# Optimization experiments

Measured on AMD Instinct MI355X. Metric: run time of the kernel, lower is better.

Reference implementation:

```python
import jax, jax.numpy as jnp
import numpy as np

B, S, H = 1, 2048, 2048
NH, NKV, HD = 32, 8, 64
RBS, ICS, RBN = 64, 64, 16          # retrieval_block_size, input_chunk_size, retrieval_block_num
RLEN = RBS * RBN                     # 1024 retrieval tokens
KV = RLEN + S                        # 3072 total kv length
START = RLEN                         # INPUT_START_IDX
SCALE = HD ** -0.5
NEG = -1e9


def _document_ids():
    # mirrors get_document_ids
    ids = np.full(KV, -1, np.int32)
    ids[:START] = np.arange(START) // RBS + 1            # retrieval blocks -> 1..RBN
    chunk = np.arange(S) // ICS
    ids[START:] = np.where(chunk == 0, -1, np.minimum(chunk, RBN))
    return ids


def _block_mask():
    # mirrors causal_retrieval_mask_mod, precomputed dense [S, KV]
    ids = _document_ids()
    qpos = np.arange(S) + START
    kv = np.arange(KV)
    causal = (qpos[:, None] >= kv[None, :]) & (kv[None, :] > START)
    doc = (ids[qpos][:, None] == ids[None, :]) & (kv[None, :] < START)
    return jnp.asarray(causal | doc)


_MASK = _block_mask()


def _rotate_half(x):
    h = x.shape[-1] // 2
    return jnp.concatenate([-x[..., h:], x[..., :h]], axis=-1)


def setup_inputs() -> dict:
    key = jax.random.key(0)
    ks = jax.random.split(key, 6)
    inv_freq = 1.0 / (10000.0 ** (np.arange(0, HD, 2, dtype=np.float32) / HD))
    ang = np.arange(S, dtype=np.float32)[:, None] * inv_freq[None, :]   # [S, HD/2]
    emb = np.concatenate([ang, ang], axis=-1)                            # [S, HD]
    cos = jnp.asarray(np.cos(emb))[None].astype(jnp.float32)            # [1, S, HD]
    sin = jnp.asarray(np.sin(emb))[None].astype(jnp.float32)
    return {
        "hidden_states": jax.random.normal(ks[0], (B, S, H), jnp.float32),
        "cos": cos,
        "sin": sin,
        "retrieval_key": jax.random.normal(ks[1], (B, NKV, RLEN, HD), jnp.float32),
        "retrieval_value": jax.random.normal(ks[2], (B, NKV, RLEN, HD), jnp.float32),
        "Wq": jax.random.normal(ks[3], (H, NH * HD), jnp.float32) * 0.02,
        "Wk": jax.random.normal(ks[4], (H, NKV * HD), jnp.float32) * 0.02,
        "Wv": jax.random.normal(ks[5], (H, NKV * HD), jnp.float32) * 0.02,
        "Wo": jax.random.normal(jax.random.fold_in(key, 7), (NH * HD, H), jnp.float32) * 0.02,
    }


def reference(hidden_states, cos, sin, retrieval_key, retrieval_value, Wq, Wk, Wv, Wo):
    # QKV projections -> [B, nheads, S, HD]
    q = (hidden_states @ Wq).reshape(B, S, NH, HD).transpose(0, 2, 1, 3)
    k = (hidden_states @ Wk).reshape(B, S, NKV, HD).transpose(0, 2, 1, 3)
    v = (hidden_states @ Wv).reshape(B, S, NKV, HD).transpose(0, 2, 1, 3)
    # RoPE (retrieval kv is pre-encoded; rope only on current tokens)
    c, s = cos[:, None, :, :], sin[:, None, :, :]
    q = q * c + _rotate_half(q) * s
    k = k * c + _rotate_half(k) * s
    # prepend retrieval kv
    k = jnp.concatenate([retrieval_key, k], axis=2)    # [B, NKV, KV, HD]
    v = jnp.concatenate([retrieval_value, v], axis=2)
    # GQA: expand kv heads
    g = NH // NKV
    k = jnp.repeat(k, g, axis=1)                        # [B, NH, KV, HD]
    v = jnp.repeat(v, g, axis=1)
    scores = jnp.einsum("bhqd,bhkd->bhqk", q, k) * SCALE
    scores = jnp.where(_MASK[None, None], scores, NEG)
    probs = jax.nn.softmax(scores, axis=-1)
    # fully-masked rows (q_idx 0) -> zero output, matching flex_attention
    row_valid = _MASK.any(axis=-1)[None, None, :, None]
    probs = jnp.where(row_valid, probs, 0.0)
    out = jnp.einsum("bhqk,bhkd->bhqd", probs, v)
    out = out.transpose(0, 2, 1, 3).reshape(B, S, NH * HD)
    return out @ Wo
```

## Files before the change

kernel.cpp:

```cpp
#include <hip/hip_runtime.h>

#define S_LEN 2048
#define H_DIM 2048
#define NH 32
#define NKV 8
#define HD 64
#define RLEN 1024
#define KVTOT 3072
#define SCALE 0.125f
#define QS 0.18033688011112042f
#define FIX8 11.541560327111707f

typedef unsigned short ushort_t;
using short8 = __attribute__((ext_vector_type(8))) short;
using f32x4 = __attribute__((ext_vector_type(4))) float;

__device__ __forceinline__ float b2f(unsigned short u) {
    union { unsigned int i; float f; } v;
    v.i = ((unsigned int)u) << 16;
    return v.f;
}
__device__ __forceinline__ unsigned short f2b(float f) {
    union { float f; unsigned int i; } v;
    v.f = f;
    unsigned int x = v.i;
    return (unsigned short)((x + 0x7fffu + ((x >> 16) & 1u)) >> 16);
}

__device__ __forceinline__ void gload16(const ushort_t* g, ushort_t* l) {
    __builtin_amdgcn_global_load_lds(
        (const __attribute__((address_space(1))) unsigned int*)g,
        (__attribute__((address_space(3))) unsigned int*)l, 16, 0, 0);
}

__device__ __forceinline__ int is_f32(const void* p) {
    const unsigned int* w = (const unsigned int*)p;
    const int lane = threadIdx.x & 63;
    int cnt = 0;
#pragma unroll
    for (int j = 0; j < 4; ++j) {
        unsigned int lo = w[lane + j * 64] & 0xFFFFu;
        unsigned int e = (lo >> 7) & 0xFFu;
        cnt += (lo != 0u && (e < 90u || e > 140u)) ? 1 : 0;
    }
    unsigned long long b = __ballot(cnt >= 2);
    return __popcll(b) > 16;
}

__global__ __launch_bounds__(256) void prep_all(
    const void* __restrict__ hs, ushort_t* __restrict__ hsb,
    const void* __restrict__ Wq, const void* __restrict__ Wk,
    const void* __restrict__ Wv, const void* __restrict__ Wo,
    ushort_t* __restrict__ WqkvT, ushort_t* __restrict__ WoT)
{
    __shared__ ushort_t S[64 * 72];
    const int id = blockIdx.x;
    if (id < 2048) {
        const int F = is_f32(hs);
        int i = (id * 256 + threadIdx.x) * 8;
        ushort_t o[8];
        if (F) {
            const float* p = (const float*)hs + i;
            float4 f0 = ((const float4*)p)[0];
            float4 f1 = ((const float4*)p)[1];
            o[0] = f2b(f0.x); o[1] = f2b(f0.y); o[2] = f2b(f0.z); o[3] = f2b(f0.w);
            o[4] = f2b(f1.x); o[5] = f2b(f1.y); o[6] = f2b(f1.z); o[7] = f2b(f1.w);
            *(uint4*)(hsb + i) = *(const uint4*)o;
        } else {
            *(uint4*)(hsb + i) = *(const uint4*)((const ushort_t*)hs + i);
        }
        return;
    }
    int z, t;
    if (id < 3072)      { z = 0; t = id - 2048; }
    else if (id < 3328) { z = 1; t = id - 3072; }
    else if (id < 3584) { z = 2; t = id - 3328; }
    else                { z = 3; t = id - 3584; }
    const void* src = (z == 0) ? Wq : (z == 1) ? Wk : (z == 2) ? Wv : Wo;
    const int F = is_f32(src);
    const int C = (z == 1 || z == 2) ? 512 : 2048;
    const int nx = (z == 1 || z == 2) ? 8 : 32;
    const int x = t % nx, y = t / nx;
    ushort_t* dst = (z == 3) ? WoT : WqkvT;
    const int rofs = (z == 1) ? 2048 : (z == 2) ? 2560 : 0;

    const int r0 = y * 64, c0 = x * 64;
    const int lr = threadIdx.x >> 2, lc = (threadIdx.x & 3) * 16;
    ushort_t tt[16];
    if (F) {
        const float* p = (const float*)src + (size_t)(r0 + lr) * C + c0 + lc;
#pragma unroll
        for (int j = 0; j < 16; j += 4) {
            float4 f = *(const float4*)(p + j);
            tt[j] = f2b(f.x); tt[j + 1] = f2b(f.y); tt[j + 2] = f2b(f.z); tt[j + 3] = f2b(f.w);
        }
    } else {
        const ushort_t* p = (const ushort_t*)src + (size_t)(r0 + lr) * C + c0 + lc;
        *(uint4*)tt = ((const uint4*)p)[0];
        *(uint4*)(tt + 8) = ((const uint4*)p)[1];
    }
    *(uint4*)&S[lr * 72 + lc] = *(const uint4*)tt;
    *(uint4*)&S[lr * 72 + lc + 8] = *(const uint4*)(tt + 8);
    __syncthreads();
    const int wc = threadIdx.x >> 2, wr = (threadIdx.x & 3) * 16;
    ushort_t o[16];
#pragma unroll
    for (int j = 0; j < 16; ++j) o[j] = S[(wr + j) * 72 + wc];
    ushort_t* q = dst + (size_t)(rofs + c0 + wc) * 2048 + r0 + wr;
    *(uint4*)q = *(const uint4*)o;
    *(uint4*)(q + 8) = *(const uint4*)(o + 8);
}

__global__ __launch_bounds__(256, 4) void gemm_qkv(
    const ushort_t* __restrict__ A, const ushort_t* __restrict__ Bt,
    ushort_t* __restrict__ C, int N, int K)
{
    __shared__ __align__(16) ushort_t As[2][64 * 32];
    __shared__ __align__(16) ushort_t Bs[2][128 * 32];
    const int tid = threadIdx.x;
    const int wave = tid >> 6, lane = tid & 63;
    const int lq = lane & 15, quad = lane >> 4;
    const int m0 = blockIdx.y * 64, n0 = blockIdx.x * 128;
    const int wm = (wave & 1) * 32, wn = (wave >> 1) * 64;
    const int nk = K >> 5;

    const int srow = wave * 16 + (lane >> 2);
    const int scol = ((lane & 3) ^ ((lane >> 3) & 3)) * 8;
    const ushort_t* ga  = A  + (size_t)(m0 + srow) * K + scol;
    const ushort_t* gb0 = Bt + (size_t)(n0 + srow) * K + scol;
    const ushort_t* gb1 = Bt + (size_t)(n0 + 64 + srow) * K + scol;
    ushort_t* lA = &As[0][0] + wave * 16 * 32;
    ushort_t* lB = &Bs[0][0] + wave * 16 * 32;
    const int rs = (lq >> 1) & 3;

    f32x4 acc[2][4];
#pragma unroll
    for (int i = 0; i < 2; ++i)
#pragma unroll
        for (int j = 0; j < 4; ++j) acc[i][j] = (f32x4){0.f, 0.f, 0.f, 0.f};

#define STAGE_G(buf, kt) do { \
        gload16(ga  + (size_t)(kt) * 32, lA + (buf) * (64 * 32)); \
        gload16(gb0 + (size_t)(kt) * 32, lB + (buf) * (128 * 32)); \
        gload16(gb1 + (size_t)(kt) * 32, lB + (buf) * (128 * 32) + 64 * 32); \
    } while (0)

    STAGE_G(0, 0);
    int cur = 0;
    for (int kt = 0; kt < nk; ++kt) {
        if (kt + 1 < nk) {
            STAGE_G(cur ^ 1, kt + 1);
            asm volatile("s_waitcnt vmcnt(3)" ::: "memory");
        } else {
            asm volatile("s_waitcnt vmcnt(0)" ::: "memory");
        }
        __builtin_amdgcn_s_barrier();
        __builtin_amdgcn_sched_barrier(0);
        short8 afr[2], bfr[4];
#pragma unroll
        for (int i = 0; i < 2; ++i)
            afr[i] = *(const short8*)&As[cur][(wm + i * 16 + lq) * 32 + (quad ^ rs) * 8];
#pragma unroll
        for (int j = 0; j < 4; ++j)
            bfr[j] = *(const short8*)&Bs[cur][(wn + j * 16 + lq) * 32 + (quad ^ rs) * 8];
#pragma unroll
        for (int i = 0; i < 2; ++i)
#pragma unroll
            for (int j = 0; j < 4; ++j)
                acc[i][j] = __builtin_amdgcn_mfma_f32_16x16x32_bf16(afr[i], bfr[j], acc[i][j], 0, 0, 0);
        __builtin_amdgcn_s_barrier();
        cur ^= 1;
    }

#pragma unroll
    for (int i = 0; i < 2; ++i)
#pragma unroll
        for (int r = 0; r < 4; ++r) {
            ushort_t* cp = C + (size_t)(m0 + wm + i * 16 + quad * 4 + r) * N + n0 + wn + lq;
#pragma unroll
            for (int j = 0; j < 4; ++j) cp[j * 16] = f2b(acc[i][j][r]);
        }
#undef STAGE_G
}

__global__ __launch_bounds__(256, 4) void gemm_fin(
    const ushort_t* __restrict__ A, const ushort_t* __restrict__ Bt,
    void* __restrict__ Cv, int N, int K, const void* __restrict__ hs)
{
    const int oF = is_f32(hs);
    __shared__ __align__(16) ushort_t As[2][64 * 32];
    __shared__ __align__(16) ushort_t Bs[2][128 * 32];
    const int tid = threadIdx.x;
    const int wave = tid >> 6, lane = tid & 63;
    const int lq = lane & 15, quad = lane >> 4;
    const int m0 = blockIdx.y * 64, n0 = blockIdx.x * 128;
    const int wm = (wave & 1) * 32, wn = (wave >> 1) * 64;
    const int nk = K >> 5;

    const int srow = wave * 16 + (lane >> 2);
    const int scol = ((lane & 3) ^ ((lane >> 3) & 3)) * 8;
    const ushort_t* ga  = A  + (size_t)(m0 + srow) * K + scol;
    const ushort_t* gb0 = Bt + (size_t)(n0 + srow) * K + scol;
    const ushort_t* gb1 = Bt + (size_t)(n0 + 64 + srow) * K + scol;
    ushort_t* lA = &As[0][0] + wave * 16 * 32;
    ushort_t* lB = &Bs[0][0] + wave * 16 * 32;
    const int rs = (lq >> 1) & 3;

    f32x4 acc[2][4];
#pragma unroll
    for (int i = 0; i < 2; ++i)
#pragma unroll
        for (int j = 0; j < 4; ++j) acc[i][j] = (f32x4){0.f, 0.f, 0.f, 0.f};

#define STAGE_G(buf, kt) do { \
        gload16(ga  + (size_t)(kt) * 32, lA + (buf) * (64 * 32)); \
        gload16(gb0 + (size_t)(kt) * 32, lB + (buf) * (128 * 32)); \
        gload16(gb1 + (size_t)(kt) * 32, lB + (buf) * (128 * 32) + 64 * 32); \
    } while (0)

    STAGE_G(0, 0);
    int cur = 0;
    for (int kt = 0; kt < nk; ++kt) {
        if (kt + 1 < nk) {
            STAGE_G(cur ^ 1, kt + 1);
            asm volatile("s_waitcnt vmcnt(3)" ::: "memory");
        } else {
            asm volatile("s_waitcnt vmcnt(0)" ::: "memory");
        }
        __builtin_amdgcn_s_barrier();
        __builtin_amdgcn_sched_barrier(0);
        short8 afr[2], bfr[4];
#pragma unroll
        for (int i = 0; i < 2; ++i)
            afr[i] = *(const short8*)&As[cur][(wm + i * 16 + lq) * 32 + (quad ^ rs) * 8];
#pragma unroll
        for (int j = 0; j < 4; ++j)
            bfr[j] = *(const short8*)&Bs[cur][(wn + j * 16 + lq) * 32 + (quad ^ rs) * 8];
#pragma unroll
        for (int i = 0; i < 2; ++i)
#pragma unroll
            for (int j = 0; j < 4; ++j)
                acc[i][j] = __builtin_amdgcn_mfma_f32_16x16x32_bf16(afr[i], bfr[j], acc[i][j], 0, 0, 0);
        __builtin_amdgcn_s_barrier();
        cur ^= 1;
    }

#pragma unroll
    for (int i = 0; i < 2; ++i)
#pragma unroll
        for (int r = 0; r < 4; ++r) {
            size_t off = (size_t)(m0 + wm + i * 16 + quad * 4 + r) * N + n0 + wn + lq;
            if (oF) {
                float* cp = (float*)Cv + off;
#pragma unroll
                for (int j = 0; j < 4; ++j) cp[j * 16] = acc[i][j][r];
            } else {
                ushort_t* cp = (ushort_t*)Cv + off;
#pragma unroll
                for (int j = 0; j < 4; ++j) cp[j * 16] = f2b(acc[i][j][r]);
            }
        }
#undef STAGE_G
}

__global__ __launch_bounds__(256) void prepKV(
    const void* __restrict__ rk, const void* __restrict__ rv,
    const ushort_t* __restrict__ qkvp,
    const void* __restrict__ cosv, const void* __restrict__ sinv,
    ushort_t* __restrict__ ktall, ushort_t* __restrict__ vtall)
{
    if (blockIdx.z == 0) {
        const int vF = is_f32(rv);
        const int t = blockIdx.x;
        const int kvh = blockIdx.y;
        __shared__ ushort_t S[64 * 72];
        const int lr = threadIdx.x >> 2, lc = (threadIdx.x & 3) * 16;
        ushort_t tt[16];
        if (t < 16) {
            size_t base = ((size_t)kvh * RLEN + t * 64 + lr) * HD + lc;
            if (vF) {
                const float* p = (const float*)rv + base;
#pragma unroll
                for (int j = 0; j < 16; j += 4) {
                    float4 f = *(const float4*)(p + j);
                    tt[j] = f2b(f.x); tt[j + 1] = f2b(f.y); tt[j + 2] = f2b(f.z); tt[j + 3] = f2b(f.w);
                }
            } else {
                const ushort_t* p = (const ushort_t*)rv + base;
                *(uint4*)tt = ((const uint4*)p)[0];
                *(uint4*)(tt + 8) = ((const uint4*)p)[1];
            }
        } else {
            const ushort_t* p = qkvp + (size_t)((t - 16) * 64 + lr) * 3072 + 2560 + kvh * HD + lc;
            *(uint4*)tt = ((const uint4*)p)[0];
            *(uint4*)(tt + 8) = ((const uint4*)p)[1];
        }
        *(uint4*)&S[lr * 72 + lc] = *(const uint4*)tt;
        *(uint4*)&S[lr * 72 + lc + 8] = *(const uint4*)(tt + 8);
        __syncthreads();
        const int wc = threadIdx.x >> 2, wr = (threadIdx.x & 3) * 16;
        ushort_t o[16];
#pragma unroll
        for (int j = 0; j < 16; ++j) o[j] = S[(wr + j) * 72 + wc];
        const int blk = t * 2 + (wr >> 5);
        ushort_t* q = vtall + (((size_t)(kvh * 96 + blk) * 64 + wc) * 32) + (wr & 31);
        *(uint4*)q = *(const uint4*)o;
        *(uint4*)(q + 8) = *(const uint4*)(o + 8);
    } else {
        const int kF = is_f32(rk), cF = is_f32(cosv), sF = is_f32(sinv);
        int flat = (blockIdx.y * 48 + blockIdx.x) * 256 + threadIdx.x;
        const int d0 = (flat & 3) * 8;
        const int p = (flat >> 2) % KVTOT;
        const int kvh = (flat >> 2) / KVTOT;
        ushort_t o0[8], o1[8];
        if (p < RLEN) {
            size_t base = ((size_t)kvh * RLEN + p) * HD;
            if (kF) {
                const float* s = (const float*)rk + base;
#pragma unroll
                for (int j = 0; j < 8; j += 4) {
                    float4 f = *(const float4*)(s + d0 + j);
                    o0[j] = f2b(f.x); o0[j + 1] = f2b(f.y); o0[j + 2] = f2b(f.z); o0[j + 3] = f2b(f.w);
                    float4 g = *(const float4*)(s + d0 + 32 + j);
                    o1[j] = f2b(g.x); o1[j + 1] = f2b(g.y); o1[j + 2] = f2b(g.z); o1[j + 3] = f2b(g.w);
                }
            } else {
                const ushort_t* s = (const ushort_t*)rk + base;
                *(uint4*)o0 = *(const uint4*)(s + d0);
                *(uint4*)o1 = *(const uint4*)(s + d0 + 32);
            }
        } else {
            const int si = p - RLEN;
            const ushort_t* s = qkvp + (size_t)si * 3072 + 2048 + kvh * HD;
            uint4 u0 = *(const uint4*)(s + d0);
            uint4 u1 = *(const uint4*)(s + d0 + 32);
            const ushort_t* a16 = (const ushort_t*)&u0;
            const ushort_t* b16 = (const ushort_t*)&u1;
            int ci = si * HD + d0;
            float c0[8], c1[8], s0[8], s1[8];
            if (cF) {
                const float* cp = (const float*)cosv + ci;
#pragma unroll
                for (int j = 0; j < 8; ++j) { c0[j] = cp[j]; c1[j] = cp[j + 32]; }
            } else {
                const ushort_t* cp = (const ushort_t*)cosv + ci;
#pragma unroll
                for (int j = 0; j < 8; ++j) { c0[j] = b2f(cp[j]); c1[j] = b2f(cp[j + 32]); }
            }
            if (sF) {
                const float* sp = (const float*)sinv + ci;
#pragma unroll
                for (int j = 0; j < 8; ++j) { s0[j] = sp[j]; s1[j] = sp[j + 32]; }
            } else {
                const ushort_t* sp = (const ushort_t*)sinv + ci;
#pragma unroll
                for (int j = 0; j < 8; ++j) { s0[j] = b2f(sp[j]); s1[j] = b2f(sp[j + 32]); }
            }
#pragma unroll
            for (int j = 0; j < 8; ++j) {
                float a = b2f(a16[j]), b = b2f(b16[j]);
                o0[j] = f2b(a * c0[j] - b * s0[j]);
                o1[j] = f2b(b * c1[j] + a * s1[j]);
            }
        }
        ushort_t* q = ktall + ((size_t)kvh * KVTOT + p) * HD;
        *(uint4*)(q + d0) = *(const uint4*)o0;
        *(uint4*)(q + d0 + 32) = *(const uint4*)o1;
    }
}

__global__ __launch_bounds__(256) void fattn(
    const ushort_t* __restrict__ qkvp, const ushort_t* __restrict__ ktall,
    const ushort_t* __restrict__ vtall, ushort_t* __restrict__ attno,
    const void* __restrict__ cosv, const void* __restrict__ sinv)
{
    const int cF = is_f32(cosv), sF = is_f32(sinv);
    const int h = blockIdx.x;
    const int yy = blockIdx.y;
    const int st = yy >> 3, r8 = yy & 7;
    const int qb = (st == 0) ? (31 - r8) : (st == 1) ? (16 + r8)
                 : (st == 2) ? (15 - r8) : r8;
    const int kvh = h >> 2;
    const int tid = threadIdx.x;
    const int wave = tid >> 6;
    const int lane = tid & 63;
    const int lq = lane & 15;
    const int quad = lane >> 4;
    const int rb64 = ((qb < 17 ? qb : 16) - 1) * 64;
    const int qrow = qb * 64 + wave * 16 + lq;

    __shared__ __align__(16) ushort_t Ks[128 * 72];
    __shared__ __align__(16) ushort_t Ps[4 * 16 * 136];
    ushort_t* pw = &Ps[wave * 16 * 136];

    short8 qfrag[2];
    {
        const int row_g = qb * 64 + wave * 16 + lq;
        const ushort_t* qrp = qkvp + (size_t)row_g * 3072 + h * HD;
        short8 t0 = *(const short8*)(qrp + quad * 8);
        short8 t1 = *(const short8*)(qrp + 32 + quad * 8);
        const int ci = row_g * HD + quad * 8;
        float c0[8], c1[8], s0[8], s1[8];
        if (cF) {
            const float* cp = (const float*)cosv + ci;
#pragma unroll
            for (int j = 0; j < 8; ++j) { c0[j] = cp[j]; c1[j] = cp[j + 32]; }
        } else {
            const ushort_t* cp = (const ushort_t*)cosv + ci;
#pragma unroll
            for (int j = 0; j < 8; ++j) { c0[j] = b2f(cp[j]); c1[j] = b2f(cp[j + 32]); }
        }
        if (sF) {
            const float* sp = (const float*)sinv + ci;
#pragma unroll
            for (int j = 0; j < 8; ++j) { s0[j] = sp[j]; s1[j] = sp[j + 32]; }
        } else {
            const ushort_t* sp = (const ushort_t*)sinv + ci;
#pragma unroll
            for (int j = 0; j < 8; ++j) { s0[j] = b2f(sp[j]); s1[j] = b2f(sp[j + 32]); }
        }
#pragma unroll
        for (int j = 0; j < 8; ++j) {
            float a = b2f((unsigned short)t0[j]), b = b2f((unsigned short)t1[j]);
            qfrag[0][j] = (short)f2b((a * c0[j] - b * s0[j]) * QS);
            qfrag[1][j] = (short)f2b((b * c1[j] + a * s1[j]) * QS);
        }
    }

    f32x4 oacc[4];
#pragma unroll
    for (int nt = 0; nt < 4; ++nt) oacc[nt] = (f32x4){0.f, 0.f, 0.f, 0.f};
    float lsum = 0.f;

    const int Lq = (qb > 0) ? qb * 64 + 128 : 64;
    const int nch = (Lq + 127) >> 7;
    const ushort_t* kbase = ktall + (size_t)kvh * KVTOT * HD;
    const ushort_t* vbase = vtall + (size_t)kvh * 96 * 2048;

    for (int c = 0; c < nch; ++c) {
        uint4 kreg0, kreg1, kreg2, kreg3;
        const int krow = tid >> 1;
        const int kd0 = (tid & 1) * 32;
        {
            int p = c * 128 + krow;
            uint4 z = {0, 0, 0, 0};
            kreg0 = z; kreg1 = z; kreg2 = z; kreg3 = z;
            if (p < Lq) {
                int pk = (qb > 0) ? ((p < 64) ? rb64 + p : 960 + p) : RLEN + p;
                const uint4* s = (const uint4*)(kbase + (size_t)pk * HD + kd0);
                kreg0 = s[0]; kreg1 = s[1]; kreg2 = s[2]; kreg3 = s[3];
            }
        }
        int vblk[4];
#pragma unroll
        for (int kc = 0; kc < 4; ++kc) {
            int p = c * 128 + kc * 32;
            int pk = (qb > 0) ? ((p < 64) ? rb64 + p : 960 + p) : RLEN + p;
            if (pk > KVTOT - 1) pk = KVTOT - 1;
            vblk[kc] = pk >> 5;
        }
        short8 vfA[4], vfB[4];
#pragma unroll
        for (int ntd = 0; ntd < 4; ++ntd)
            vfA[ntd] = *(const short8*)(vbase + ((size_t)vblk[0] * 64 + ntd * 16 + lq) * 32 + quad * 8);
#pragma unroll
        for (int ntd = 0; ntd < 4; ++ntd)
            vfB[ntd] = *(const short8*)(vbase + ((size_t)vblk[1] * 64 + ntd * 16 + lq) * 32 + quad * 8);

        {
            uint4* dk = (uint4*)&Ks[krow * 72 + kd0];
            dk[0] = kreg0; dk[1] = kreg1; dk[2] = kreg2; dk[3] = kreg3;
        }
        __syncthreads();

        const bool lastc = (c == nch - 1) || (qb == 0);
#pragma unroll
        for (int nt = 0; nt < 8; ++nt) {
            f32x4 a = (f32x4){0.f, 0.f, 0.f, 0.f};
            a = __builtin_amdgcn_mfma_f32_16x16x32_bf16(
                *(const short8*)&Ks[(nt * 16 + lq) * 72 + quad * 8], qfrag[0], a, 0, 0, 0);
            a = __builtin_amdgcn_mfma_f32_16x16x32_bf16(
                *(const short8*)&Ks[(nt * 16 + lq) * 72 + 32 + quad * 8], qfrag[1], a, 0, 0, 0);
            float pex[4];
#pragma unroll
            for (int rr = 0; rr < 4; ++rr) {
                const int p = c * 128 + nt * 16 + quad * 4 + rr;
                float pexp = exp2f(a[rr] - FIX8);
                if (lastc) {
                    bool valid;
                    if (qb > 0) valid = (p < 64) || ((p - 64) >= 1 && (p - 64) <= qrow);
                    else        valid = (p >= 1 && p <= qrow);
                    if (!valid) pexp = 0.f;
                } else if (c == 0) {
                    if (p == 64) pexp = 0.f;
                }
                lsum += pexp;
                pex[rr] = pexp;
            }
            unsigned int w0, w1;
            asm("v_cvt_pk_bf16_f32 %0, %1, %2" : "=v"(w0) : "v"(pex[0]), "v"(pex[1]));
            asm("v_cvt_pk_bf16_f32 %0, %1, %2" : "=v"(w1) : "v"(pex[2]), "v"(pex[3]));
            *(uint2*)&pw[lq * 136 + nt * 16 + quad * 4] = make_uint2(w0, w1);
        }

#pragma unroll
        for (int kc = 0; kc < 4; ++kc) {
            short8 pa = *(const short8*)&pw[lq * 136 + kc * 32 + quad * 8];
            short8 vf0, vf1, vf2, vf3;
            if (kc == 0)      { vf0 = vfA[0]; vf1 = vfA[1]; vf2 = vfA[2]; vf3 = vfA[3]; }
            else if (kc == 1) { vf0 = vfB[0]; vf1 = vfB[1]; vf2 = vfB[2]; vf3 = vfB[3]; }
            else {
                const int b = vblk[kc];
                vf0 = *(const short8*)(vbase + ((size_t)b * 64 + 0 * 16 + lq) * 32 + quad * 8);
                vf1 = *(const short8*)(vbase + ((size_t)b * 64 + 1 * 16 + lq) * 32 + quad * 8);
                vf2 = *(const short8*)(vbase + ((size_t)b * 64 + 2 * 16 + lq) * 32 + quad * 8);
                vf3 = *(const short8*)(vbase + ((size_t)b * 64 + 3 * 16 + lq) * 32 + quad * 8);
            }
            oacc[0] = __builtin_amdgcn_mfma_f32_16x16x32_bf16(pa, vf0, oacc[0], 0, 0, 0);
            oacc[1] = __builtin_amdgcn_mfma_f32_16x16x32_bf16(pa, vf1, oacc[1], 0, 0, 0);
            oacc[2] = __builtin_amdgcn_mfma_f32_16x16x32_bf16(pa, vf2, oacc[2], 0, 0, 0);
            oacc[3] = __builtin_amdgcn_mfma_f32_16x16x32_bf16(pa, vf3, oacc[3], 0, 0, 0);
        }
        __syncthreads();
    }

    float tot = lsum;
    tot += __shfl_xor(tot, 16, 64);
    tot += __shfl_xor(tot, 32, 64);
#pragma unroll
    for (int rr = 0; rr < 4; ++rr) {
        const int qg = qb * 64 + wave * 16 + quad * 4 + rr;
        const float tr = __shfl(tot, quad * 4 + rr, 64);
        const float inv = (qg == 0) ? 0.f : 1.f / tr;
        ushort_t* orow = attno + (size_t)qg * 2048 + h * HD;
#pragma unroll
        for (int nt = 0; nt < 4; ++nt)
            orow[nt * 16 + lq] = f2b(oacc[nt][rr] * inv);
    }
}

extern "C" void kernel_launch(void* const* d_in, const int* in_sizes, int n_in,
                              void* d_out, int out_size, void* d_ws, size_t ws_size,
                              hipStream_t stream) {
    const void* hs   = d_in[0];
    const void* cosv = d_in[1];
    const void* sinv = d_in[2];
    const void* rk   = d_in[3];
    const void* rv   = d_in[4];
    const void* Wq   = d_in[5];
    const void* Wk   = d_in[6];
    const void* Wv   = d_in[7];
    const void* Wo   = d_in[8];

    char* ws = (char*)d_ws;
    ushort_t* hsb    = (ushort_t*)(ws + (1u  << 20));
    ushort_t* ktall  = hsb;
    ushort_t* vtall  = (ushort_t*)(ws + (1u << 20) + (13u << 18));
    ushort_t* WqkvT  = (ushort_t*)(ws + (9u  << 20));
    ushort_t* attno  = WqkvT;
    ushort_t* WoT    = (ushort_t*)(ws + (21u << 20));
    ushort_t* qkvp   = (ushort_t*)(ws + (29u << 20));

    prep_all<<<4608, 256, 0, stream>>>(hs, hsb, Wq, Wk, Wv, Wo, WqkvT, WoT);

    gemm_qkv<<<dim3(3072 / 128, 2048 / 64), 256, 0, stream>>>(hsb, WqkvT, qkvp, 3072, 2048);

    prepKV<<<dim3(48, 8, 2), 256, 0, stream>>>(rk, rv, qkvp, cosv, sinv, ktall, vtall);

    fattn<<<dim3(NH, 32), 256, 0, stream>>>(qkvp, ktall, vtall, attno, cosv, sinv);

    gemm_fin<<<dim3(2048 / 128, 2048 / 64), 256, 0, stream>>>(attno, WoT, d_out, 2048, 2048, hs);
}
```

Baseline: 256.5 us.

## Fuse hidden-state conversion and K/V RoPE packing into QKV GEMM, drop prepKV

The separate hidden-state bf16 conversion pass is removed. The QKV GEMM now loads the fp32 activations directly through registers and converts them before writing to LDS. Its epilogue applies RoPE to K and writes K and V straight into the attention-ready ktall/vtall layouts. Retrieval K/V conversion moves into prep_all, eliminating one kernel launch and the qkvp round trip for K/V. In exchange, A-tile loads are no longer asynchronous direct-to-LDS and the epilogue does strided scalar stores plus cos/sin loads.

```diff
diff --git a/kernel.cpp b/kernel.cpp
--- a/kernel.cpp
+++ b/kernel.cpp
@@ -48,73 +48,112 @@
 }
 
 __global__ __launch_bounds__(256) void prep_all(
-    const void* __restrict__ hs, ushort_t* __restrict__ hsb,
+    const void* __restrict__ rk, const void* __restrict__ rv,
     const void* __restrict__ Wq, const void* __restrict__ Wk,
     const void* __restrict__ Wv, const void* __restrict__ Wo,
-    ushort_t* __restrict__ WqkvT, ushort_t* __restrict__ WoT)
+    ushort_t* __restrict__ WqkvT, ushort_t* __restrict__ WoT,
+    ushort_t* __restrict__ ktall, ushort_t* __restrict__ vtall)
 {
     __shared__ ushort_t S[64 * 72];
     const int id = blockIdx.x;
-    if (id < 2048) {
-        const int F = is_f32(hs);
-        int i = (id * 256 + threadIdx.x) * 8;
-        ushort_t o[8];
+    if (id < 2560) {
+        int z, t;
+        if (id < 1024)      { z = 0; t = id; }
+        else if (id < 1280) { z = 1; t = id - 1024; }
+        else if (id < 1536) { z = 2; t = id - 1280; }
+        else                { z = 3; t = id - 1536; }
+        const void* src = (z == 0) ? Wq : (z == 1) ? Wk : (z == 2) ? Wv : Wo;
+        const int F = is_f32(src);
+        const int C = (z == 1 || z == 2) ? 512 : 2048;
+        const int nx = (z == 1 || z == 2) ? 8 : 32;
+        const int x = t % nx, y = t / nx;
+        ushort_t* dst = (z == 3) ? WoT : WqkvT;
+        const int rofs = (z == 1) ? 2048 : (z == 2) ? 2560 : 0;
+
+        const int r0 = y * 64, c0 = x * 64;
+        const int lr = threadIdx.x >> 2, lc = (threadIdx.x & 3) * 16;
+        ushort_t tt[16];
         if (F) {
-            const float* p = (const float*)hs + i;
+            const float* p = (const float*)src + (size_t)(r0 + lr) * C + c0 + lc;
+#pragma unroll
+            for (int j = 0; j < 16; j += 4) {
+                float4 f = *(const float4*)(p + j);
+                tt[j] = f2b(f.x); tt[j + 1] = f2b(f.y); tt[j + 2] = f2b(f.z); tt[j + 3] = f2b(f.w);
+            }
+        } else {
+            const ushort_t* p = (const ushort_t*)src + (size_t)(r0 + lr) * C + c0 + lc;
+            *(uint4*)tt = ((const uint4*)p)[0];
+            *(uint4*)(tt + 8) = ((const uint4*)p)[1];
+        }
+        *(uint4*)&S[lr * 72 + lc] = *(const uint4*)tt;
+        *(uint4*)&S[lr * 72 + lc + 8] = *(const uint4*)(tt + 8);
+        __syncthreads();
+        const int wc = threadIdx.x >> 2, wr = (threadIdx.x & 3) * 16;
+        ushort_t o[16];
+#pragma unroll
+        for (int j = 0; j < 16; ++j) o[j] = S[(wr + j) * 72 + wc];
+        ushort_t* q = dst + (size_t)(rofs + c0 + wc) * 2048 + r0 + wr;
+        *(uint4*)q = *(const uint4*)o;
+        *(uint4*)(q + 8) = *(const uint4*)(o + 8);
+    } else if (id < 2816) {
+        const int kF = is_f32(rk);
+        const int e = ((id - 2560) * 256 + threadIdx.x) * 8;
+        const int kvh = e >> 16;
+        const int rem = e & 65535;
+        ushort_t* dst = ktall + (size_t)kvh * (KVTOT * 64) + rem;
+        if (kF) {
+            const float* p = (const float*)rk + e;
             float4 f0 = ((const float4*)p)[0];
             float4 f1 = ((const float4*)p)[1];
+            ushort_t o[8];
             o[0] = f2b(f0.x); o[1] = f2b(f0.y); o[2] = f2b(f0.z); o[3] = f2b(f0.w);
             o[4] = f2b(f1.x); o[5] = f2b(f1.y); o[6] = f2b(f1.z); o[7] = f2b(f1.w);
-            *(uint4*)(hsb + i) = *(const uint4*)o;
-        } else {
-            *(uint4*)(hsb + i) = *(const uint4*)((const ushort_t*)hs + i);
-        }
-        return;
-    }
-    int z, t;
-    if (id < 3072)      { z = 0; t = id - 2048; }
-    else if (id < 3328) { z = 1; t = id - 3072; }
-    else if (id < 3584) { z = 2; t = id - 3328; }
-    else                { z = 3; t = id - 3584; }
-    const void* src = (z == 0) ? Wq : (z == 1) ? Wk : (z == 2) ? Wv : Wo;
-    const int F = is_f32(src);
-    const int C = (z == 1 || z == 2) ? 512 : 2048;
-    const int nx = (z == 1 || z == 2) ? 8 : 32;
-    const int x = t % nx, y = t / nx;
-    ushort_t* dst = (z == 3) ? WoT : WqkvT;
-    const int rofs = (z == 1) ? 2048 : (z == 2) ? 2560 : 0;
-
-    const int r0 = y * 64, c0 = x * 64;
-    const int lr = threadIdx.x >> 2, lc = (threadIdx.x & 3) * 16;
-    ushort_t tt[16];
-    if (F) {
-        const float* p = (const float*)src + (size_t)(r0 + lr) * C + c0 + lc;
-#pragma unroll
-        for (int j = 0; j < 16; j += 4) {
-            float4 f = *(const float4*)(p + j);
-            tt[j] = f2b(f.x); tt[j + 1] = f2b(f.y); tt[j + 2] = f2b(f.z); tt[j + 3] = f2b(f.w);
+            *(uint4*)dst = *(const uint4*)o;
+        } else {
+            *(uint4*)dst = *(const uint4*)((const ushort_t*)rk + e);
         }
     } else {
-        const ushort_t* p = (const ushort_t*)src + (size_t)(r0 + lr) * C + c0 + lc;
-        *(uint4*)tt = ((const uint4*)p)[0];
-        *(uint4*)(tt + 8) = ((const uint4*)p)[1];
-    }
-    *(uint4*)&S[lr * 72 + lc] = *(const uint4*)tt;
-    *(uint4*)&S[lr * 72 + lc + 8] = *(const uint4*)(tt + 8);
-    __syncthreads();
-    const int wc = threadIdx.x >> 2, wr = (threadIdx.x & 3) * 16;
-    ushort_t o[16];
-#pragma unroll
-    for (int j = 0; j < 16; ++j) o[j] = S[(wr + j) * 72 + wc];
-    ushort_t* q = dst + (size_t)(rofs + c0 + wc) * 2048 + r0 + wr;
-    *(uint4*)q = *(const uint4*)o;
-    *(uint4*)(q + 8) = *(const uint4*)(o + 8);
+        const int idv = id - 2816;
+        const int t = idv & 15;
+        const int kvh = idv >> 4;
+        const int vF = is_f32(rv);
+        const int lr = threadIdx.x >> 2, lc = (threadIdx.x & 3) * 16;
+        ushort_t tt[16];
+        size_t base = ((size_t)kvh * RLEN + t * 64 + lr) * HD + lc;
+        if (vF) {
+            const float* p = (const float*)rv + base;
+#pragma unroll
+            for (int j = 0; j < 16; j += 4) {
+                float4 f = *(const float4*)(p + j);
+                tt[j] = f2b(f.x); tt[j + 1] = f2b(f.y); tt[j + 2] = f2b(f.z); tt[j + 3] = f2b(f.w);
+            }
+        } else {
+            const ushort_t* p = (const ushort_t*)rv + base;
+            *(uint4*)tt = ((const uint4*)p)[0];
+            *(uint4*)(tt + 8) = ((const uint4*)p)[1];
+        }
+        *(uint4*)&S[lr * 72 + lc] = *(const uint4*)tt;
+        *(uint4*)&S[lr * 72 + lc + 8] = *(const uint4*)(tt + 8);
+        __syncthreads();
+        const int wc = threadIdx.x >> 2, wr = (threadIdx.x & 3) * 16;
+        ushort_t o[16];
+#pragma unroll
+        for (int j = 0; j < 16; ++j) o[j] = S[(wr + j) * 72 + wc];
+        const int blk = t * 2 + (wr >> 5);
+        ushort_t* q = vtall + (((size_t)(kvh * 96 + blk) * 64 + wc) * 32) + (wr & 31);
+        *(uint4*)q = *(const uint4*)o;
+        *(uint4*)(q + 8) = *(const uint4*)(o + 8);
+    }
 }
 
 __global__ __launch_bounds__(256, 4) void gemm_qkv(
-    const ushort_t* __restrict__ A, const ushort_t* __restrict__ Bt,
-    ushort_t* __restrict__ C, int N, int K)
+    const void* __restrict__ hs, const ushort_t* __restrict__ Bt,
+    ushort_t* __restrict__ qkvp, ushort_t* __restrict__ ktall,
+    ushort_t* __restrict__ vtall,
+    const void* __restrict__ cosv, const void* __restrict__ sinv)
 {
+    const int K = 2048;
+    const int aF = is_f32(hs);
     __shared__ __align__(16) ushort_t As[2][64 * 32];
     __shared__ __align__(16) ushort_t Bs[2][128 * 32];
     const int tid = threadIdx.x;
@@ -124,35 +163,55 @@
     const int wm = (wave & 1) * 32, wn = (wave >> 1) * 64;
     const int nk = K >> 5;
 
+    const int ar = tid >> 2, ag = tid & 3;
+    const int aslot = (ag ^ ((ar >> 1) & 3)) * 8;
+    const float*    apf = (const float*)hs    + (size_t)(m0 + ar) * K + ag * 8;
+    const ushort_t* aph = (const ushort_t*)hs + (size_t)(m0 + ar) * K + ag * 8;
     const int srow = wave * 16 + (lane >> 2);
     const int scol = ((lane & 3) ^ ((lane >> 3) & 3)) * 8;
-    const ushort_t* ga  = A  + (size_t)(m0 + srow) * K + scol;
     const ushort_t* gb0 = Bt + (size_t)(n0 + srow) * K + scol;
     const ushort_t* gb1 = Bt + (size_t)(n0 + 64 + srow) * K + scol;
-    ushort_t* lA = &As[0][0] + wave * 16 * 32;
     ushort_t* lB = &Bs[0][0] + wave * 16 * 32;
     const int rs = (lq >> 1) & 3;
 
-    f32x4 acc[2][4];
-#pragma unroll
-    for (int i = 0; i < 2; ++i)
-#pragma unroll
-        for (int j = 0; j < 4; ++j) acc[i][j] = (f32x4){0.f, 0.f, 0.f, 0.f};
-
-#define STAGE_G(buf, kt) do { \
-        gload16(ga  + (size_t)(kt) * 32, lA + (buf) * (64 * 32)); \
+    float4 af0, af1;
+    uint2 au0, au1;
+
+#define ALOAD(kt) do { \
+        if (aF) { af0 = *(const float4*)(apf + (size_t)(kt) * 32); \
+                  af1 = *(const float4*)(apf + (size_t)(kt) * 32 + 4); } \
+        else    { au0 = *(const uint2*)(aph + (size_t)(kt) * 32); \
+                  au1 = *(const uint2*)(aph + (size_t)(kt) * 32 + 4); } \
+    } while (0)
+#define AWRITE(buf) do { \
+        ushort_t t8[8]; \
+        if (aF) { t8[0]=f2b(af0.x); t8[1]=f2b(af0.y); t8[2]=f2b(af0.z); t8[3]=f2b(af0.w); \
+                  t8[4]=f2b(af1.x); t8[5]=f2b(af1.y); t8[6]=f2b(af1.z); t8[7]=f2b(af1.w); } \
+        else    { *(uint2*)t8 = au0; *(uint2*)(t8 + 4) = au1; } \
+        *(uint4*)&As[buf][ar * 32 + aslot] = *(const uint4*)t8; \
+    } while (0)
+#define GLOADB(buf, kt) do { \
         gload16(gb0 + (size_t)(kt) * 32, lB + (buf) * (128 * 32)); \
         gload16(gb1 + (size_t)(kt) * 32, lB + (buf) * (128 * 32) + 64 * 32); \
     } while (0)
 
-    STAGE_G(0, 0);
+    f32x4 acc[2][4];
+#pragma unroll
+    for (int i = 0; i < 2; ++i)
+#pragma unroll
+        for (int j = 0; j < 4; ++j) acc[i][j] = (f32x4){0.f, 0.f, 0.f, 0.f};
+
+    ALOAD(0); AWRITE(0);
+    GLOADB(0, 0);
     int cur = 0;
     for (int kt = 0; kt < nk; ++kt) {
-        if (kt + 1 < nk) {
-            STAGE_G(cur ^ 1, kt + 1);
-            asm volatile("s_waitcnt vmcnt(3)" ::: "memory");
-        } else {
-            asm volatile("s_waitcnt vmcnt(0)" ::: "memory");
+        const bool more = (kt + 1 < nk);
+        if (more) {
+            ALOAD(kt + 1);
+            GLOADB(cur ^ 1, kt + 1);
+            asm volatile("s_waitcnt vmcnt(4) lgkmcnt(0)" ::: "memory");
+        } else {
+            asm volatile("s_waitcnt vmcnt(0) lgkmcnt(0)" ::: "memory");
         }
         __builtin_amdgcn_s_barrier();
         __builtin_amdgcn_sched_barrier(0);
@@ -168,19 +227,70 @@
 #pragma unroll
             for (int j = 0; j < 4; ++j)
                 acc[i][j] = __builtin_amdgcn_mfma_f32_16x16x32_bf16(afr[i], bfr[j], acc[i][j], 0, 0, 0);
+        if (more) AWRITE(cur ^ 1);
         __builtin_amdgcn_s_barrier();
         cur ^= 1;
     }
-
-#pragma unroll
-    for (int i = 0; i < 2; ++i)
-#pragma unroll
-        for (int r = 0; r < 4; ++r) {
-            ushort_t* cp = C + (size_t)(m0 + wm + i * 16 + quad * 4 + r) * N + n0 + wn + lq;
-#pragma unroll
-            for (int j = 0; j < 4; ++j) cp[j * 16] = f2b(acc[i][j][r]);
-        }
-#undef STAGE_G
+#undef ALOAD
+#undef AWRITE
+#undef GLOADB
+
+    if (n0 < 2048) {
+#pragma unroll
+        for (int i = 0; i < 2; ++i)
+#pragma unroll
+            for (int r = 0; r < 4; ++r) {
+                ushort_t* cp = qkvp + (size_t)(m0 + wm + i * 16 + quad * 4 + r) * 2048 + n0 + wn + lq;
+#pragma unroll
+                for (int j = 0; j < 4; ++j) cp[j * 16] = f2b(acc[i][j][r]);
+            }
+    } else if (n0 < 2560) {
+        const int cF = is_f32(cosv), sF = is_f32(sinv);
+        const int kvh = (n0 - 2048 + wn) >> 6;
+#pragma unroll
+        for (int i = 0; i < 2; ++i)
+#pragma unroll
+            for (int r = 0; r < 4; ++r) {
+                const int si = m0 + wm + i * 16 + quad * 4 + r;
+                const int ci = si * HD + lq;
+                float c0, c1, c2, c3, s0, s1, s2, s3;
+                if (cF) {
+                    const float* cp = (const float*)cosv + ci;
+                    c0 = cp[0]; c1 = cp[16]; c2 = cp[32]; c3 = cp[48];
+                } else {
+                    const ushort_t* cp = (const ushort_t*)cosv + ci;
+                    c0 = b2f(cp[0]); c1 = b2f(cp[16]); c2 = b2f(cp[32]); c3 = b2f(cp[48]);
+                }
+                if (sF) {
+                    const float* sp = (const float*)sinv + ci;
+                    s0 = sp[0]; s1 = sp[16]; s2 = sp[32]; s3 = sp[48];
+                } else {
+                    const ushort_t* sp = (const ushort_t*)sinv + ci;
+                    s0 = b2f(sp[0]); s1 = b2f(sp[16]); s2 = b2f(sp[32]); s3 = b2f(sp[48]);
+                }
+                ushort_t* kp = ktall + ((size_t)kvh * KVTOT + RLEN + si) * HD + lq;
+                kp[0]  = f2b(acc[i][0][r] * c0 - acc[i][2][r] * s0);
+                kp[16] = f2b(acc[i][1][r] * c1 - acc[i][3][r] * s1);
+                kp[32] = f2b(acc[i][2][r] * c2 + acc[i][0][r] * s2);
+                kp[48] = f2b(acc[i][3][r] * c3 + acc[i][1][r] * s3);
+            }
+    } else {
+        const int kvh = (n0 - 2560 + wn) >> 6;
+#pragma unroll
+        for (int i = 0; i < 2; ++i) {
+            const int si0 = m0 + wm + i * 16 + quad * 4;
+            const int blk = 32 + (si0 >> 5);
+            const int slot = si0 & 31;
+#pragma unroll
+            for (int j = 0; j < 4; ++j) {
+                const int d = j * 16 + lq;
+                ushort_t o[4];
+#pragma unroll
+                for (int r = 0; r < 4; ++r) o[r] = f2b(acc[i][j][r]);
+                *(uint2*)(vtall + ((size_t)(kvh * 96 + blk) * 64 + d) * 32 + slot) = *(const uint2*)o;
+            }
+        }
+    }
 }
 
 __global__ __launch_bounds__(256, 4) void gemm_fin(
@@ -261,112 +371,6 @@
             }
         }
 #undef STAGE_G
-}
-
-__global__ __launch_bounds__(256) void prepKV(
-    const void* __restrict__ rk, const void* __restrict__ rv,
-    const ushort_t* __restrict__ qkvp,
-    const void* __restrict__ cosv, const void* __restrict__ sinv,
-    ushort_t* __restrict__ ktall, ushort_t* __restrict__ vtall)
-{
-    if (blockIdx.z == 0) {
-        const int vF = is_f32(rv);
-        const int t = blockIdx.x;
-        const int kvh = blockIdx.y;
-        __shared__ ushort_t S[64 * 72];
-        const int lr = threadIdx.x >> 2, lc = (threadIdx.x & 3) * 16;
-        ushort_t tt[16];
-        if (t < 16) {
-            size_t base = ((size_t)kvh * RLEN + t * 64 + lr) * HD + lc;
-            if (vF) {
-                const float* p = (const float*)rv + base;
-#pragma unroll
-                for (int j = 0; j < 16; j += 4) {
-                    float4 f = *(const float4*)(p + j);
-                    tt[j] = f2b(f.x); tt[j + 1] = f2b(f.y); tt[j + 2] = f2b(f.z); tt[j + 3] = f2b(f.w);
-                }
-            } else {
-                const ushort_t* p = (const ushort_t*)rv + base;
-                *(uint4*)tt = ((const uint4*)p)[0];
-                *(uint4*)(tt + 8) = ((const uint4*)p)[1];
-            }
-        } else {
-            const ushort_t* p = qkvp + (size_t)((t - 16) * 64 + lr) * 3072 + 2560 + kvh * HD + lc;
-            *(uint4*)tt = ((const uint4*)p)[0];
-            *(uint4*)(tt + 8) = ((const uint4*)p)[1];
-        }
-        *(uint4*)&S[lr * 72 + lc] = *(const uint4*)tt;
-        *(uint4*)&S[lr * 72 + lc + 8] = *(const uint4*)(tt + 8);
-        __syncthreads();
-        const int wc = threadIdx.x >> 2, wr = (threadIdx.x & 3) * 16;
-        ushort_t o[16];
-#pragma unroll
-        for (int j = 0; j < 16; ++j) o[j] = S[(wr + j) * 72 + wc];
-        const int blk = t * 2 + (wr >> 5);
-        ushort_t* q = vtall + (((size_t)(kvh * 96 + blk) * 64 + wc) * 32) + (wr & 31);
-        *(uint4*)q = *(const uint4*)o;
-        *(uint4*)(q + 8) = *(const uint4*)(o + 8);
-    } else {
-        const int kF = is_f32(rk), cF = is_f32(cosv), sF = is_f32(sinv);
-        int flat = (blockIdx.y * 48 + blockIdx.x) * 256 + threadIdx.x;
-        const int d0 = (flat & 3) * 8;
-        const int p = (flat >> 2) % KVTOT;
-        const int kvh = (flat >> 2) / KVTOT;
-        ushort_t o0[8], o1[8];
-        if (p < RLEN) {
-            size_t base = ((size_t)kvh * RLEN + p) * HD;
-            if (kF) {
-                const float* s = (const float*)rk + base;
-#pragma unroll
-                for (int j = 0; j < 8; j += 4) {
-                    float4 f = *(const float4*)(s + d0 + j);
-                    o0[j] = f2b(f.x); o0[j + 1] = f2b(f.y); o0[j + 2] = f2b(f.z); o0[j + 3] = f2b(f.w);
-                    float4 g = *(const float4*)(s + d0 + 32 + j);
-                    o1[j] = f2b(g.x); o1[j + 1] = f2b(g.y); o1[j + 2] = f2b(g.z); o1[j + 3] = f2b(g.w);
-                }
-            } else {
-                const ushort_t* s = (const ushort_t*)rk + base;
-                *(uint4*)o0 = *(const uint4*)(s + d0);
-                *(uint4*)o1 = *(const uint4*)(s + d0 + 32);
-            }
-        } else {
-            const int si = p - RLEN;
-            const ushort_t* s = qkvp + (size_t)si * 3072 + 2048 + kvh * HD;
-            uint4 u0 = *(const uint4*)(s + d0);
-            uint4 u1 = *(const uint4*)(s + d0 + 32);
-            const ushort_t* a16 = (const ushort_t*)&u0;
-            const ushort_t* b16 = (const ushort_t*)&u1;
-            int ci = si * HD + d0;
-            float c0[8], c1[8], s0[8], s1[8];
-            if (cF) {
-                const float* cp = (const float*)cosv + ci;
-#pragma unroll
-                for (int j = 0; j < 8; ++j) { c0[j] = cp[j]; c1[j] = cp[j + 32]; }
-            } else {
-                const ushort_t* cp = (const ushort_t*)cosv + ci;
-#pragma unroll
-                for (int j = 0; j < 8; ++j) { c0[j] = b2f(cp[j]); c1[j] = b2f(cp[j + 32]); }
-            }
-            if (sF) {
-                const float* sp = (const float*)sinv + ci;
-#pragma unroll
-                for (int j = 0; j < 8; ++j) { s0[j] = sp[j]; s1[j] = sp[j + 32]; }
-            } else {
-                const ushort_t* sp = (const ushort_t*)sinv + ci;
-#pragma unroll
-                for (int j = 0; j < 8; ++j) { s0[j] = b2f(sp[j]); s1[j] = b2f(sp[j + 32]); }
-            }
-#pragma unroll
-            for (int j = 0; j < 8; ++j) {
-                float a = b2f(a16[j]), b = b2f(b16[j]);
-                o0[j] = f2b(a * c0[j] - b * s0[j]);
-                o1[j] = f2b(b * c1[j] + a * s1[j]);
-            }
-        }
-        ushort_t* q = ktall + ((size_t)kvh * KVTOT + p) * HD;
-        *(uint4*)(q + d0) = *(const uint4*)o0;
-        *(uint4*)(q + d0 + 32) = *(const uint4*)o1;
-    }
 }
 
 __global__ __launch_bounds__(256) void fattn(
@@ -396,7 +400,7 @@
     short8 qfrag[2];
     {
         const int row_g = qb * 64 + wave * 16 + lq;
-        const ushort_t* qrp = qkvp + (size_t)row_g * 3072 + h * HD;
+        const ushort_t* qrp = qkvp + (size_t)row_g * 2048 + h * HD;
         short8 t0 = *(const short8*)(qrp + quad * 8);
         short8 t1 = *(const short8*)(qrp + 32 + quad * 8);
         const int ci = row_g * HD + quad * 8;
@@ -553,21 +557,18 @@
     const void* Wo   = d_in[8];
 
     char* ws = (char*)d_ws;
-    ushort_t* hsb    = (ushort_t*)(ws + (1u  << 20));
-    ushort_t* ktall  = hsb;
-    ushort_t* vtall  = (ushort_t*)(ws + (1u << 20) + (13u << 18));
-    ushort_t* WqkvT  = (ushort_t*)(ws + (9u  << 20));
-    ushort_t* attno  = WqkvT;
-    ushort_t* WoT    = (ushort_t*)(ws + (21u << 20));
-    ushort_t* qkvp   = (ushort_t*)(ws + (29u << 20));
-
-    prep_all<<<4608, 256, 0, stream>>>(hs, hsb, Wq, Wk, Wv, Wo, WqkvT, WoT);
-
-    gemm_qkv<<<dim3(3072 / 128, 2048 / 64), 256, 0, stream>>>(hsb, WqkvT, qkvp, 3072, 2048);
-
-    prepKV<<<dim3(48, 8, 2), 256, 0, stream>>>(rk, rv, qkvp, cosv, sinv, ktall, vtall);
+    ushort_t* ktall = (ushort_t*)ws;
+    ushort_t* vtall = (ushort_t*)(ws + (3u  << 20));
+    ushort_t* WqkvT = (ushort_t*)(ws + (6u  << 20));
+    ushort_t* WoT   = (ushort_t*)(ws + (18u << 20));
+    ushort_t* qkvp  = (ushort_t*)(ws + (26u << 20));
+    ushort_t* attno = WqkvT;
+
+    prep_all<<<2944, 256, 0, stream>>>(rk, rv, Wq, Wk, Wv, Wo, WqkvT, WoT, ktall, vtall);
+
+    gemm_qkv<<<dim3(24, 32), 256, 0, stream>>>(hs, WqkvT, qkvp, ktall, vtall, cosv, sinv);
 
     fattn<<<dim3(NH, 32), 256, 0, stream>>>(qkvp, ktall, vtall, attno, cosv, sinv);
 
-    gemm_fin<<<dim3(2048 / 128, 2048 / 64), 256, 0, stream>>>(attno, WoT, d_out, 2048, 2048, hs);
-}
+    gemm_fin<<<dim3(16, 32), 256, 0, stream>>>(attno, WoT, d_out, 2048, 2048, hs);
+}
```

Measured after the change: 270.3 us. 5.4% more time.
